# Kernel tuning notes

Measured on AMD Instinct MI355X. Metric: run time of the kernel, lower is better.

## Reference

```python
import jax, jax.numpy as jnp
import numpy as np

N = 50000
E = 800000
DZ = 64
DH = 64


def setup_inputs() -> dict:
    key = jax.random.key(0)
    ks = jax.random.split(key, 10)
    z = jax.random.normal(ks[0], (N, DZ), dtype=jnp.float32)
    edge_src = jax.random.randint(ks[1], (E,), 0, N, dtype=jnp.int32)
    edge_dst = jax.random.randint(ks[2], (E,), 0, N, dtype=jnp.int32)
    # weights: normal(0, 0.1); biases: uniform(-0.1, 0.1) as in the torch init
    W_cur = 0.1 * jax.random.normal(ks[3], (DH, DZ), dtype=jnp.float32)
    b_cur = jax.random.uniform(ks[4], (DH,), minval=-0.1, maxval=0.1, dtype=jnp.float32)
    W_nbr = 0.1 * jax.random.normal(ks[5], (DH, 2 * DZ), dtype=jnp.float32)
    b_nbr = jax.random.uniform(ks[6], (DH,), minval=-0.1, maxval=0.1, dtype=jnp.float32)
    W_out = 0.1 * jax.random.normal(ks[7], (DZ, 2 * DH), dtype=jnp.float32)
    b_out = jax.random.uniform(ks[8], (DZ,), minval=-0.1, maxval=0.1, dtype=jnp.float32)
    return {"z": z, "edge_src": edge_src, "edge_dst": edge_dst,
            "W_cur": W_cur, "b_cur": b_cur, "W_nbr": W_nbr, "b_nbr": b_nbr,
            "W_out": W_out, "b_out": b_out}


def reference(z, edge_src, edge_dst, W_cur, b_cur, W_nbr, b_nbr, W_out, b_out):
    # self branch: Sigmoid(Linear(dim_z -> dim_h))  [N, DH]
    curvv = jax.nn.sigmoid(z @ W_cur.T + b_cur)
    # per-edge: concat(z[center], z[neighbor]) -> Sigmoid(Linear)  [E, DH]
    e = jnp.concatenate([z[edge_dst], z[edge_src]], axis=-1)  # [E, 2*DZ]
    m = jax.nn.sigmoid(e @ W_nbr.T + b_nbr)
    # sum-aggregate messages per center node (isolated nodes -> zeros)
    nbrvv = jax.ops.segment_sum(m, edge_dst, num_segments=N)  # [N, DH]
    # fuse: Tanh(Linear(concat(cur, nbr) -> dim_z))
    h = jnp.concatenate([curvv, nbrvv], axis=-1)  # [N, 2*DH]
    dzdt = jnp.tanh(h @ W_out.T + b_out)
    return dzdt
```

## Files before the change

kernel.cpp:

```cpp
#include <hip/hip_runtime.h>
#include <math.h>

#define NN 50000
#define NE 800000
#define BSH 7
#define NBUCK 391
#define CAP 4096
#define CHUNK 4096
#define NCH ((NE + CHUNK - 1) / CHUNK)
#define K1B 782
#define EPT2 8
#define GSZ 24

typedef float4 f4;
typedef float2 f2;
typedef unsigned short u16;
typedef unsigned int u32;

__device__ __forceinline__ float sigf(float x) {
    return __builtin_amdgcn_rcpf(1.0f + __expf(-x));
}

__device__ __forceinline__ u16 f32_to_bf16_rne(float f) {
    unsigned u = __float_as_uint(f);
    u += 0x7FFFu + ((u >> 16) & 1u);
    return (u16)(u >> 16);
}

#define K1_WFLOATS (3 * 32 * 64 * 2)
__global__ __launch_bounds__(512, 4) void k1_sc(
    const float* __restrict__ z,
    const float* __restrict__ Wc, const float* __restrict__ bc,
    const float* __restrict__ Wn, const float* __restrict__ bn,
    float* __restrict__ P, u16* __restrict__ Qh, float* __restrict__ C,
    const int* __restrict__ esrc, const int* __restrict__ edst,
    int* __restrict__ gcur, u32* __restrict__ ebuf)
{
    const int tid = threadIdx.x;
    if (blockIdx.x < K1B) {
        __shared__ float sh[K1_WFLOATS + 8 * 256];
        f2* w2 = (f2*)sh;
        for (int j = tid; j < 3 * 32 * 64; j += 512) {
            const int m = j >> 11, r = j & 2047;
            const int k2 = r >> 6, h = r & 63;
            const float* s = (m == 0) ? (Wc + h * 64 + 2 * k2)
                                      : (Wn + h * 128 + (m - 1) * 64 + 2 * k2);
            w2[(m * 32 + k2) * 64 + h] = *(const f2*)s;
        }
        __syncthreads();

        const int lane = tid & 63;
        const int wid  = tid >> 6;
        f4* tile = (f4*)(sh + K1_WFLOATS) + wid * 64;
        const f2* wl0 = w2;
        const f2* wl1 = w2 + 32 * 64;
        const f2* wl2 = w2 + 2 * 32 * 64;
        const float bcur = bc[lane], bnbr = bn[lane];

        const int gw = blockIdx.x * 8 + wid;
        const int nw = K1B * 8;
        for (int chunk = gw; chunk < NN / 4; chunk += nw) {
            const int n0 = chunk * 4;
            tile[lane] = *(const f4*)(z + n0 * 64 + lane * 4);
            float a0[4], a1[4], a2[4];
            #pragma unroll
            for (int ni = 0; ni < 4; ++ni) { a0[ni] = 0.f; a1[ni] = 0.f; a2[ni] = 0.f; }
            #pragma unroll 2
            for (int k4 = 0; k4 < 16; ++k4) {
                const f2 w0a = wl0[(2 * k4) * 64 + lane], w0b = wl0[(2 * k4 + 1) * 64 + lane];
                const f2 w1a = wl1[(2 * k4) * 64 + lane], w1b = wl1[(2 * k4 + 1) * 64 + lane];
                const f2 w2a = wl2[(2 * k4) * 64 + lane], w2b = wl2[(2 * k4 + 1) * 64 + lane];
                #pragma unroll
                for (int ni = 0; ni < 4; ++ni) {
                    const f4 zz = tile[ni * 16 + k4];
                    a0[ni] = fmaf(w0b.y, zz.w, fmaf(w0b.x, zz.z, fmaf(w0a.y, zz.y, fmaf(w0a.x, zz.x, a0[ni]))));
                    a1[ni] = fmaf(w1b.y, zz.w, fmaf(w1b.x, zz.z, fmaf(w1a.y, zz.y, fmaf(w1a.x, zz.x, a1[ni]))));
                    a2[ni] = fmaf(w2b.y, zz.w, fmaf(w2b.x, zz.z, fmaf(w2a.y, zz.y, fmaf(w2a.x, zz.x, a2[ni]))));
                }
            }
            #pragma unroll
            for (int ni = 0; ni < 4; ++ni) {
                const int n = n0 + ni;
                C[n * 64 + lane]  = sigf(a0[ni] + bcur);
                P[n * 64 + lane]  = a1[ni] + bnbr;
                Qh[n * 64 + lane] = f32_to_bf16_rne(a2[ni]);
            }
        }
    } else {
        __shared__ int cnt[NBUCK];
        __shared__ int gbase[NBUCK];
        __shared__ int lcur[NBUCK];
        for (int i = tid; i < NBUCK; i += 512) cnt[i] = 0;
        __syncthreads();

        const int base = (blockIdx.x - K1B) * CHUNK;
        u32 ent[EPT2];
        int nb[EPT2];
        #pragma unroll
        for (int t = 0; t < EPT2; ++t) {
            const int e = base + t * 512 + tid;
            if (e < NE) {
                const int d = edst[e], s = esrc[e];
                const int b = d >> BSH;
                ent[t] = ((u32)(d & 127) << 16) | (u32)s;
                nb[t] = b;
                atomicAdd(&cnt[b], 1);
            } else {
                nb[t] = -1;
            }
        }
        __syncthreads();
        for (int i = tid; i < NBUCK; i += 512) {
            gbase[i] = cnt[i] ? atomicAdd(&gcur[i], cnt[i]) : 0;
            lcur[i] = 0;
        }
        __syncthreads();
        #pragma unroll
        for (int t = 0; t < EPT2; ++t) {
            if (nb[t] >= 0) {
                const int li = atomicAdd(&lcur[nb[t]], 1);
                ebuf[nb[t] * CAP + gbase[nb[t]] + li] = ent[t];
            }
        }
    }
}

__global__ __launch_bounds__(256) void k_bsort(const int* __restrict__ gcur,
                                               const u32* __restrict__ ebuf,
                                               u32* __restrict__ bd,
                                               u16* __restrict__ ss)
{
    __shared__ int hist[128];
    __shared__ int lcur[128];
    __shared__ int ps[128];
    __shared__ int tot;
    const int b = blockIdx.x;
    const int ecnt = gcur[b];
    const int e0 = b * CAP;
    const int n0 = b << BSH;
    const int t = threadIdx.x;

    if (t < 128) hist[t] = 0;
    __syncthreads();
    for (int j = t; j < ecnt; j += 256)
        atomicAdd(&hist[(ebuf[e0 + j] >> 16) & 127], 1);
    __syncthreads();
    if (t < 128) ps[t] = (hist[t] + 7) & ~7;
    __syncthreads();
    for (int o = 1; o < 128; o <<= 1) {
        int v = 0;
        if (t < 128 && t >= o) v = ps[t - o];
        __syncthreads();
        if (t < 128 && t >= o) ps[t] += v;
        __syncthreads();
    }
    if (t < 128) {
        const int a = hist[t];
        const int r = (a + 7) & ~7;
        const int excl = ps[t] - r;
        lcur[t] = excl;
        const int n = n0 + t;
        if (n < NN) bd[n] = ((u32)(e0 + excl) << 8) | (u32)a;
        if (t == 127) tot = ps[127];
    }
    __syncthreads();
    const int zw = (tot + 32) >> 1;
    u32* ssw = (u32*)(ss + e0);
    for (int j = t; j < zw; j += 256) ssw[j] = 0;
    __syncthreads();
    for (int j = t; j < ecnt; j += 256) {
        const u32 ent = ebuf[e0 + j];
        const int p = atomicAdd(&lcur[(ent >> 16) & 127], 1);
        ss[e0 + p] = (u16)(ent & 0xFFFFu);
    }
}

__global__ __launch_bounds__(256) void k2_agg(
    const u32* __restrict__ bd, const u16* __restrict__ ss,
    const float* __restrict__ P, const u16* __restrict__ Qh,
    float* __restrict__ NB)
{
    const int lane = threadIdx.x & 63;
    const int n = blockIdx.x * 4 + (threadIdx.x >> 6);
    if (n >= NN) return;
    const u32 w = bd[n];
    const int beg = __builtin_amdgcn_readfirstlane((int)(w >> 8));
    const int dg  = __builtin_amdgcn_readfirstlane((int)(w & 255u));
    const u16* qbl = Qh + lane;
    const float p = P[n * 64 + lane];
    float acc = 0.f;

    for (int jb = 0; jb < dg; jb += GSZ) {
        const u16* ip = ss + beg + jb;
        uint4 iv0, iv1, iv2;
        asm volatile("global_load_dwordx4 %0, %1, off" : "=v"(iv0) : "v"(ip));
        asm volatile("global_load_dwordx4 %0, %1, off offset:16" : "=v"(iv1) : "v"(ip));
        asm volatile("global_load_dwordx4 %0, %1, off offset:32" : "=v"(iv2) : "v"(ip));
        asm volatile("s_waitcnt vmcnt(0)" ::: "memory");
        __builtin_amdgcn_sched_barrier(0);
        const u32 wv[12] = {iv0.x, iv0.y, iv0.z, iv0.w,
                            iv1.x, iv1.y, iv1.z, iv1.w,
                            iv2.x, iv2.y, iv2.z, iv2.w};
        u32 q[GSZ];
        #pragma unroll
        for (int t8 = 0; t8 < 12; ++t8) {
            const u16* aL = qbl + ((wv[t8] & 0xFFFFu) << 6);
            const u16* aH = qbl + ((wv[t8] >> 16) << 6);
            asm volatile("global_load_ushort %0, %1, off" : "=v"(q[2 * t8])     : "v"(aL));
            asm volatile("global_load_ushort %0, %1, off" : "=v"(q[2 * t8 + 1]) : "v"(aH));
        }
        asm volatile("s_waitcnt vmcnt(0)" ::: "memory");
        __builtin_amdgcn_sched_barrier(0);
        #pragma unroll
        for (int t = 0; t < GSZ; ++t) {
            const float m = sigf(p + __uint_as_float(q[t] << 16));
            acc += (jb + t < dg) ? m : 0.f;
        }
    }
    NB[n * 64 + lane] = acc;
}

#define K3_WFLOATS (64 * 64 * 2)
__global__ __launch_bounds__(512, 4) void k3_out(
    const float* __restrict__ C, const float* __restrict__ NB,
    const float* __restrict__ Wo, const float* __restrict__ bo,
    float* __restrict__ out)
{
    __shared__ float sh[K3_WFLOATS + 8 * 512];
    const int tid = threadIdx.x;
    f2* w2 = (f2*)sh;
    for (int j = tid; j < 64 * 64; j += 512) {
        const int k2 = j >> 6, d = j & 63;
        w2[k2 * 64 + d] = *(const f2*)(Wo + d * 128 + 2 * k2);
    }
    __syncthreads();

    const int lane = tid & 63;
    const int wid  = tid >> 6;
    f4* tile = (f4*)(sh + K3_WFLOATS) + wid * 128;
    const float bout = bo[lane];

    const int gw = blockIdx.x * 8 + wid;
    const int nw = gridDim.x * 8;
    for (int chunk = gw; chunk < NN / 4; chunk += nw) {
        const int n0 = chunk * 4;
        #pragma unroll
        for (int tt = 0; tt < 2; ++tt) {
            const int j = lane + tt * 64;
            const int ni = j >> 5, q = j & 31;
            const float* src = (q < 16) ? (C + (n0 + ni) * 64 + q * 4)
                                        : (NB + (n0 + ni) * 64 + (q - 16) * 4);
            tile[ni * 32 + q] = *(const f4*)src;
        }
        float acc[4];
        #pragma unroll
        for (int ni = 0; ni < 4; ++ni) acc[ni] = 0.f;
        #pragma unroll 2
        for (int k4 = 0; k4 < 32; ++k4) {
            const f2 wa = w2[(2 * k4) * 64 + lane];
            const f2 wb = w2[(2 * k4 + 1) * 64 + lane];
            #pragma unroll
            for (int ni = 0; ni < 4; ++ni) {
                const f4 hv = tile[ni * 32 + k4];
                acc[ni] = fmaf(wb.y, hv.w, fmaf(wb.x, hv.z, fmaf(wa.y, hv.y, fmaf(wa.x, hv.x, acc[ni]))));
            }
        }
        #pragma unroll
        for (int ni = 0; ni < 4; ++ni)
            out[(n0 + ni) * 64 + lane] = tanhf(acc[ni] + bout);
    }
}

extern "C" void kernel_launch(void* const* d_in, const int* in_sizes, int n_in,
                              void* d_out, int out_size, void* d_ws, size_t ws_size,
                              hipStream_t stream) {
    const float* z  = (const float*)d_in[0];
    const int* esrc = (const int*)d_in[1];
    const int* edst = (const int*)d_in[2];
    const float* Wc = (const float*)d_in[3];
    const float* bc = (const float*)d_in[4];
    const float* Wn = (const float*)d_in[5];
    const float* bn = (const float*)d_in[6];
    const float* Wo = (const float*)d_in[7];
    const float* bo = (const float*)d_in[8];
    float* out = (float*)d_out;

    float* P   = (float*)d_ws;
    float* C   = P + (size_t)NN * 64;
    float* NB  = C + (size_t)NN * 64;
    u16* Qh    = (u16*)(NB + (size_t)NN * 64);
    u32* bd    = (u32*)(Qh + (size_t)NN * 64);
    int* gcur  = (int*)(bd + NN + 64);
    u32* ebuf  = (u32*)(gcur + 512);
    u16* ss    = (u16*)(ebuf + (size_t)NBUCK * CAP);

    hipMemsetAsync(gcur, 0, 512 * sizeof(int), stream);
    k1_sc<<<K1B + NCH, 512, 0, stream>>>(z, Wc, bc, Wn, bn, P, Qh, C,
                                         esrc, edst, gcur, ebuf);
    k_bsort<<<NBUCK, 256, 0, stream>>>(gcur, ebuf, bd, ss);
    k2_agg<<<12500, 256, 0, stream>>>(bd, ss, P, Qh, NB);
    k3_out<<<782, 512, 0, stream>>>(C, NB, Wo, bo, out);
}
```

Baseline: 114.4 us.

## Fuse neighbor aggregation and output linear layer into one kernel

Merges the per-node edge aggregation kernel and the output matmul+tanh kernel into one kernel. Each wave aggregates four nodes and writes the C and aggregated vectors straight into shared memory, which removes the NB buffer round trip through global memory and one launch. It also splits the edge loop into full groups with no masking plus one masked tail group, and widens the zero padding of the sorted index array. In exchange the gather-heavy aggregation now runs with the larger shared-memory footprint and 512-thread blocks of the matmul stage. That may lower occupancy and latency hiding for the random gathers.

```diff
diff --git a/kernel.cpp b/kernel.cpp
--- a/kernel.cpp
+++ b/kernel.cpp
@@ -164,7 +164,7 @@
         if (t == 127) tot = ps[127];
     }
     __syncthreads();
-    const int zw = (tot + 32) >> 1;
+    const int zw = (tot + 48) >> 1;
     u32* ssw = (u32*)(ss + e0);
     for (int j = t; j < zw; j += 256) ssw[j] = 0;
     __syncthreads();
@@ -175,58 +175,14 @@
     }
 }
 
-__global__ __launch_bounds__(256) void k2_agg(
+#define KF_WFLOATS (64 * 64 * 2)
+__global__ __launch_bounds__(512) void k23(
     const u32* __restrict__ bd, const u16* __restrict__ ss,
     const float* __restrict__ P, const u16* __restrict__ Qh,
-    float* __restrict__ NB)
+    const float* __restrict__ C, const float* __restrict__ Wo,
+    const float* __restrict__ bo, float* __restrict__ out)
 {
-    const int lane = threadIdx.x & 63;
-    const int n = blockIdx.x * 4 + (threadIdx.x >> 6);
-    if (n >= NN) return;
-    const u32 w = bd[n];
-    const int beg = __builtin_amdgcn_readfirstlane((int)(w >> 8));
-    const int dg  = __builtin_amdgcn_readfirstlane((int)(w & 255u));
-    const u16* qbl = Qh + lane;
-    const float p = P[n * 64 + lane];
-    float acc = 0.f;
-
-    for (int jb = 0; jb < dg; jb += GSZ) {
-        const u16* ip = ss + beg + jb;
-        uint4 iv0, iv1, iv2;
-        asm volatile("global_load_dwordx4 %0, %1, off" : "=v"(iv0) : "v"(ip));
-        asm volatile("global_load_dwordx4 %0, %1, off offset:16" : "=v"(iv1) : "v"(ip));
-        asm volatile("global_load_dwordx4 %0, %1, off offset:32" : "=v"(iv2) : "v"(ip));
-        asm volatile("s_waitcnt vmcnt(0)" ::: "memory");
-        __builtin_amdgcn_sched_barrier(0);
-        const u32 wv[12] = {iv0.x, iv0.y, iv0.z, iv0.w,
-                            iv1.x, iv1.y, iv1.z, iv1.w,
-                            iv2.x, iv2.y, iv2.z, iv2.w};
-        u32 q[GSZ];
-        #pragma unroll
-        for (int t8 = 0; t8 < 12; ++t8) {
-            const u16* aL = qbl + ((wv[t8] & 0xFFFFu) << 6);
-            const u16* aH = qbl + ((wv[t8] >> 16) << 6);
-            asm volatile("global_load_ushort %0, %1, off" : "=v"(q[2 * t8])     : "v"(aL));
-            asm volatile("global_load_ushort %0, %1, off" : "=v"(q[2 * t8 + 1]) : "v"(aH));
-        }
-        asm volatile("s_waitcnt vmcnt(0)" ::: "memory");
-        __builtin_amdgcn_sched_barrier(0);
-        #pragma unroll
-        for (int t = 0; t < GSZ; ++t) {
-            const float m = sigf(p + __uint_as_float(q[t] << 16));
-            acc += (jb + t < dg) ? m : 0.f;
-        }
-    }
-    NB[n * 64 + lane] = acc;
-}
-
-#define K3_WFLOATS (64 * 64 * 2)
-__global__ __launch_bounds__(512, 4) void k3_out(
-    const float* __restrict__ C, const float* __restrict__ NB,
-    const float* __restrict__ Wo, const float* __restrict__ bo,
-    float* __restrict__ out)
-{
-    __shared__ float sh[K3_WFLOATS + 8 * 512];
+    __shared__ float sh[KF_WFLOATS + 8 * 512];
     const int tid = threadIdx.x;
     f2* w2 = (f2*)sh;
     for (int j = tid; j < 64 * 64; j += 512) {
@@ -237,37 +193,93 @@
 
     const int lane = tid & 63;
     const int wid  = tid >> 6;
-    f4* tile = (f4*)(sh + K3_WFLOATS) + wid * 128;
+    float* tile = sh + KF_WFLOATS + wid * 512;
+    const f4* t4 = (const f4*)tile;
+    const u16* qbl = Qh + lane;
     const float bout = bo[lane];
 
-    const int gw = blockIdx.x * 8 + wid;
-    const int nw = gridDim.x * 8;
-    for (int chunk = gw; chunk < NN / 4; chunk += nw) {
+    for (int chunk = blockIdx.x * 8 + wid; chunk < NN / 4; chunk += gridDim.x * 8) {
         const int n0 = chunk * 4;
         #pragma unroll
-        for (int tt = 0; tt < 2; ++tt) {
-            const int j = lane + tt * 64;
-            const int ni = j >> 5, q = j & 31;
-            const float* src = (q < 16) ? (C + (n0 + ni) * 64 + q * 4)
-                                        : (NB + (n0 + ni) * 64 + (q - 16) * 4);
-            tile[ni * 32 + q] = *(const f4*)src;
-        }
-        float acc[4];
-        #pragma unroll
-        for (int ni = 0; ni < 4; ++ni) acc[ni] = 0.f;
+        for (int i = 0; i < 4; ++i) {
+            const int n = n0 + i;
+            const u32 w = bd[n];
+            const int beg = __builtin_amdgcn_readfirstlane((int)(w >> 8));
+            const int dg  = __builtin_amdgcn_readfirstlane((int)(w & 255u));
+            const float p = P[n * 64 + lane];
+            tile[i * 128 + lane] = C[n * 64 + lane];
+            float acc = 0.f;
+
+            int jb = 0;
+            for (; jb + GSZ <= dg; jb += GSZ) {
+                const u16* ip = ss + beg + jb;
+                uint4 iv0, iv1, iv2;
+                asm volatile("global_load_dwordx4 %0, %1, off" : "=v"(iv0) : "v"(ip));
+                asm volatile("global_load_dwordx4 %0, %1, off offset:16" : "=v"(iv1) : "v"(ip));
+                asm volatile("global_load_dwordx4 %0, %1, off offset:32" : "=v"(iv2) : "v"(ip));
+                asm volatile("s_waitcnt vmcnt(0)" ::: "memory");
+                __builtin_amdgcn_sched_barrier(0);
+                const u32 wv[12] = {iv0.x, iv0.y, iv0.z, iv0.w,
+                                    iv1.x, iv1.y, iv1.z, iv1.w,
+                                    iv2.x, iv2.y, iv2.z, iv2.w};
+                u32 q[GSZ];
+                #pragma unroll
+                for (int t8 = 0; t8 < 12; ++t8) {
+                    const u16* aL = qbl + ((wv[t8] & 0xFFFFu) << 6);
+                    const u16* aH = qbl + ((wv[t8] >> 16) << 6);
+                    asm volatile("global_load_ushort %0, %1, off" : "=v"(q[2 * t8])     : "v"(aL));
+                    asm volatile("global_load_ushort %0, %1, off" : "=v"(q[2 * t8 + 1]) : "v"(aH));
+                }
+                asm volatile("s_waitcnt vmcnt(0)" ::: "memory");
+                __builtin_amdgcn_sched_barrier(0);
+                #pragma unroll
+                for (int t = 0; t < GSZ; ++t)
+                    acc += sigf(p + __uint_as_float(q[t] << 16));
+            }
+            if (jb < dg) {
+                const u16* ip = ss + beg + jb;
+                uint4 iv0, iv1, iv2;
+                asm volatile("global_load_dwordx4 %0, %1, off" : "=v"(iv0) : "v"(ip));
+                asm volatile("global_load_dwordx4 %0, %1, off offset:16" : "=v"(iv1) : "v"(ip));
+                asm volatile("global_load_dwordx4 %0, %1, off offset:32" : "=v"(iv2) : "v"(ip));
+                asm volatile("s_waitcnt vmcnt(0)" ::: "memory");
+                __builtin_amdgcn_sched_barrier(0);
+                const u32 wv[12] = {iv0.x, iv0.y, iv0.z, iv0.w,
+                                    iv1.x, iv1.y, iv1.z, iv1.w,
+                                    iv2.x, iv2.y, iv2.z, iv2.w};
+                u32 q[GSZ];
+                #pragma unroll
+                for (int t8 = 0; t8 < 12; ++t8) {
+                    const u16* aL = qbl + ((wv[t8] & 0xFFFFu) << 6);
+                    const u16* aH = qbl + ((wv[t8] >> 16) << 6);
+                    asm volatile("global_load_ushort %0, %1, off" : "=v"(q[2 * t8])     : "v"(aL));
+                    asm volatile("global_load_ushort %0, %1, off" : "=v"(q[2 * t8 + 1]) : "v"(aH));
+                }
+                asm volatile("s_waitcnt vmcnt(0)" ::: "memory");
+                __builtin_amdgcn_sched_barrier(0);
+                #pragma unroll
+                for (int t = 0; t < GSZ; ++t) {
+                    const float m = sigf(p + __uint_as_float(q[t] << 16));
+                    acc += (jb + t < dg) ? m : 0.f;
+                }
+            }
+            tile[i * 128 + 64 + lane] = acc;
+        }
+
+        float a2[4] = {0.f, 0.f, 0.f, 0.f};
         #pragma unroll 2
         for (int k4 = 0; k4 < 32; ++k4) {
             const f2 wa = w2[(2 * k4) * 64 + lane];
             const f2 wb = w2[(2 * k4 + 1) * 64 + lane];
             #pragma unroll
-            for (int ni = 0; ni < 4; ++ni) {
-                const f4 hv = tile[ni * 32 + k4];
-                acc[ni] = fmaf(wb.y, hv.w, fmaf(wb.x, hv.z, fmaf(wa.y, hv.y, fmaf(wa.x, hv.x, acc[ni]))));
+            for (int i = 0; i < 4; ++i) {
+                const f4 hv = t4[i * 32 + k4];
+                a2[i] = fmaf(wb.y, hv.w, fmaf(wb.x, hv.z, fmaf(wa.y, hv.y, fmaf(wa.x, hv.x, a2[i]))));
             }
         }
         #pragma unroll
-        for (int ni = 0; ni < 4; ++ni)
-            out[(n0 + ni) * 64 + lane] = tanhf(acc[ni] + bout);
+        for (int i = 0; i < 4; ++i)
+            out[(n0 + i) * 64 + lane] = tanhf(a2[i] + bout);
     }
 }
 
@@ -287,8 +299,7 @@
 
     float* P   = (float*)d_ws;
     float* C   = P + (size_t)NN * 64;
-    float* NB  = C + (size_t)NN * 64;
-    u16* Qh    = (u16*)(NB + (size_t)NN * 64);
+    u16* Qh    = (u16*)(C + (size_t)NN * 64);
     u32* bd    = (u32*)(Qh + (size_t)NN * 64);
     int* gcur  = (int*)(bd + NN + 64);
     u32* ebuf  = (u32*)(gcur + 512);
@@ -298,6 +309,5 @@
     k1_sc<<<K1B + NCH, 512, 0, stream>>>(z, Wc, bc, Wn, bn, P, Qh, C,
                                          esrc, edst, gcur, ebuf);
     k_bsort<<<NBUCK, 256, 0, stream>>>(gcur, ebuf, bd, ss);
-    k2_agg<<<12500, 256, 0, stream>>>(bd, ss, P, Qh, NB);
-    k3_out<<<782, 512, 0, stream>>>(C, NB, Wo, bo, out);
-}
+    k23<<<1563, 512, 0, stream>>>(bd, ss, P, Qh, C, Wo, bo, out);
+}
```

Measured after the change: 111.5 us. 1.03x faster.
